# Kernel tuning notes

Measured on AMD Instinct MI355X. Metric: run time of the kernel, lower is better.

## Reference

```python
import jax, jax.numpy as jnp
import numpy as np

LEAF = 32
N = 262144          # num_nodes, power of 2
NLEV = 8            # HODLR levels
RANK = 16           # off-diagonal low-rank
NNZ = 1310720       # ~5 nnz per row


def setup_inputs() -> dict:
    key = jax.random.key(0)
    ks = jax.random.split(key, 24)
    inp = {}
    inp["leaf_blocks"] = jax.random.normal(ks[0], (1, N // LEAF, LEAF, LEAF), jnp.float32) * 0.1
    for l in range(NLEV):
        inp[f"u{l}"] = jax.random.normal(ks[1 + 2 * l], (1, N, RANK), jnp.float32) * 0.05
        inp[f"v{l}"] = jax.random.normal(ks[2 + 2 * l], (1, N, RANK), jnp.float32) * 0.05
    inp["A_indices"] = jax.random.randint(ks[17], (2, NNZ), 0, N, dtype=jnp.int32).astype(jnp.int64)
    inp["A_values"] = jax.random.normal(ks[18], (NNZ,), jnp.float32)
    inp["z"] = jax.random.normal(ks[19], (1, N, 1), jnp.float32)
    inp["num_nodes"] = N
    return inp


def apply_hodlr(leaf_blocks, factors, x, leaf_size=LEAF):
    # x: [B, n, 1]; leaf_blocks: [B, n/leaf, leaf, leaf]
    B, n, _ = x.shape
    nb = n // leaf_size
    xb = x.reshape(B, nb, leaf_size, 1)
    L = leaf_blocks
    # y = L @ (L^T @ x) + 1e-4 * x  per leaf block
    yb = jnp.matmul(L, jnp.matmul(jnp.swapaxes(L, -1, -2), xb)) + xb * 1e-4
    y = yb.reshape(B, n, 1)
    for li, (u, v) in enumerate(factors):
        num_splits = 2 ** (li + 1)
        bs = n // num_splits
        if bs == 0:
            continue
        npair = num_splits // 2
        vl = npair * 2 * bs  # == n for power-of-2 n
        xv = x[:, :vl].reshape(B, npair, 2, bs, 1)
        uv = u[:, :vl].reshape(B, npair, 2, bs, -1)
        vv = v[:, :vl].reshape(B, npair, 2, bs, -1)
        xL, xR = xv[:, :, 0], xv[:, :, 1]
        uL, uR = uv[:, :, 0], uv[:, :, 1]
        vL, vR = vv[:, :, 0], vv[:, :, 1]
        # cross-block low-rank updates: y_L += U_L (V_R^T x_R), y_R += U_R (V_L^T x_L)
        yL = jnp.matmul(uL, jnp.matmul(jnp.swapaxes(vR, -1, -2), xR))
        yR = jnp.matmul(uR, jnp.matmul(jnp.swapaxes(vL, -1, -2), xL))
        upd = jnp.stack([yL, yR], axis=2).reshape(B, vl, 1)
        if vl < n:
            upd = jnp.pad(upd, ((0, 0), (0, n - vl), (0, 0)))
        y = y + upd
    return y


def reference(leaf_blocks, u0, v0, u1, v1, u2, v2, u3, v3, u4, v4, u5, v5, u6, v6, u7, v7,
              A_indices, A_values, z, num_nodes):
    factors = [(u0, v0), (u1, v1), (u2, v2), (u3, v3),
               (u4, v4), (u5, v5), (u6, v6), (u7, v7)]
    w = apply_hodlr(leaf_blocks, factors, z)           # [1, N, 1]
    w_flat = w[0, :, 0]                                 # [N]
    rows, cols = A_indices[0], A_indices[1]
    # sparse COO matvec: y[r] = sum_k A_values[k] * w[cols[k]] over rows
    y_flat = jax.ops.segment_sum(A_values * w_flat[cols], rows, num_segments=num_nodes)
    y = y_flat.reshape(1, num_nodes, 1)
    return jnp.mean((y - z) ** 2)
```

## Files before the change

### kernel.cpp

```cpp
#include <hip/hip_runtime.h>

#define NN 262144
#define RANK 16
#define NNZ_K 1310720

struct P8 { const float* p[8]; };

__global__ __launch_bounds__(256) void k_levels_t(P8 v, const float* __restrict__ z,
                                                  float* __restrict__ tg) {
    __shared__ float zl[512];
    __shared__ float red[8][4][16];
    const int tid  = threadIdx.x;
    const int base = blockIdx.x * 512;

    zl[tid]       = z[base + tid];
    zl[tid + 256] = z[base + tid + 256];
    __syncthreads();

    const int q = tid & 3;
    const int e = tid >> 2;

    float4 acc[8];
#pragma unroll
    for (int l = 0; l < 8; ++l) acc[l] = make_float4(0.f, 0.f, 0.f, 0.f);

#pragma unroll
    for (int it = 0; it < 8; ++it) {
        const int jloc = it * 64 + e;
        const size_t j = (size_t)(base + jloc);
        const float zz = zl[jloc];
#pragma unroll
        for (int l = 0; l < 8; ++l) {
            const float4 vv = *(const float4*)(v.p[l] + j * RANK + q * 4);
            acc[l].x += vv.x * zz;
            acc[l].y += vv.y * zz;
            acc[l].z += vv.z * zz;
            acc[l].w += vv.w * zz;
        }
    }

    const int lane = tid & 63;
    const int wv   = tid >> 6;
#pragma unroll
    for (int l = 0; l < 8; ++l) {
        float4 a = acc[l];
#pragma unroll
        for (int m = 4; m <= 32; m <<= 1) {
            a.x += __shfl_xor(a.x, m);
            a.y += __shfl_xor(a.y, m);
            a.z += __shfl_xor(a.z, m);
            a.w += __shfl_xor(a.w, m);
        }
        if (lane < 4) *(float4*)&red[l][wv][lane * 4] = a;
    }
    __syncthreads();

    if (tid < 128) {
        const int l = tid >> 4;
        const int r = tid & 15;
        const float s = red[l][0][r] + red[l][1][r] + red[l][2][r] + red[l][3][r];
        const int h = base >> (17 - l);
        atomicAdd(&tg[(((2 << l) - 2) + h) * 16 + r], s);
    }
}

__global__ __launch_bounds__(256) void k_apply(const float* __restrict__ leaf, P8 u,
                                               const float* __restrict__ z,
                                               const float* __restrict__ tg,
                                               float* __restrict__ w) {
    __shared__ float Lp[8 * 1056];
    __shared__ float xl[256];
    __shared__ float t32[8][32];
    __shared__ float tl[8][16];

    const int tid  = threadIdx.x;
    const int base = blockIdx.x * 256;

    const float4* Lg = (const float4*)(leaf + (size_t)base * 32);
#pragma unroll
    for (int k = 0; k < 8; ++k) {
        const int fi = tid + k * 256;
        const float4 val = Lg[fi];
        const int lb  = fi >> 8;
        const int off = (fi & 255) * 4;
        const int row = off >> 5;
        const int col = off & 31;
        float* d = &Lp[lb * 1056 + row * 33 + col];
        d[0] = val.x; d[1] = val.y; d[2] = val.z; d[3] = val.w;
    }
    xl[tid] = z[base + tid];
    if (tid < 128) {
        const int l = tid >> 4;
        const int r = tid & 15;
        const int h = base >> (17 - l);
        tl[l][r] = tg[(((2 << l) - 2) + (h ^ 1)) * 16 + r];
    }
    __syncthreads();

    {
        const int lb = tid >> 5;
        const int c  = tid & 31;
        const float* Lb = &Lp[lb * 1056];
        const float* xb = &xl[lb * 32];
        float s = 0.f;
#pragma unroll
        for (int row = 0; row < 32; ++row)
            s += Lb[row * 33 + c] * xb[row];
        t32[lb][c] = s;
    }
    __syncthreads();

    {
        const int lb = tid >> 5;
        const int r  = tid & 31;
        const float* Lb = &Lp[lb * 1056 + r * 33];
        float acc = 1e-4f * xl[tid];
#pragma unroll
        for (int c = 0; c < 32; ++c)
            acc += Lb[c] * t32[lb][c];

        const size_t i = (size_t)(base + tid);
#pragma unroll
        for (int l = 0; l < 8; ++l) {
            const float4* up = (const float4*)(u.p[l] + i * RANK);
            const float4 a0 = up[0], a1 = up[1], a2 = up[2], a3 = up[3];
            acc += a0.x * tl[l][0]  + a0.y * tl[l][1]  + a0.z * tl[l][2]  + a0.w * tl[l][3]
                 + a1.x * tl[l][4]  + a1.y * tl[l][5]  + a1.z * tl[l][6]  + a1.w * tl[l][7]
                 + a2.x * tl[l][8]  + a2.y * tl[l][9]  + a2.z * tl[l][10] + a2.w * tl[l][11]
                 + a3.x * tl[l][12] + a3.y * tl[l][13] + a3.z * tl[l][14] + a3.w * tl[l][15];
        }
        w[i] = acc;
    }
}

__global__ __launch_bounds__(256) void k_spmv(const int* __restrict__ idx,
                                              const float* __restrict__ vals,
                                              const float* __restrict__ w,
                                              float* __restrict__ y) {
    const int k = blockIdx.x * 256 + threadIdx.x;
    const int row = idx[k];
    const int col = idx[NNZ_K + k];
    atomicAdd(&y[row], vals[k] * w[col]);
}

__global__ __launch_bounds__(256) void k_loss(const float* __restrict__ y,
                                              const float* __restrict__ z,
                                              float* __restrict__ loss) {
    const int i = blockIdx.x * 256 + threadIdx.x;
    const float d = y[i] - z[i];
    float s = d * d;
#pragma unroll
    for (int m = 32; m >= 1; m >>= 1) s += __shfl_down(s, m);
    __shared__ float r4[4];
    const int lane = threadIdx.x & 63, wv = threadIdx.x >> 6;
    if (lane == 0) r4[wv] = s;
    __syncthreads();
    if (threadIdx.x == 0) atomicAdd(loss, r4[0] + r4[1] + r4[2] + r4[3]);
}

__global__ void k_fin(const float* __restrict__ loss, float* __restrict__ out) {
    out[0] = loss[0] * (1.0f / (float)NN);
}

extern "C" void kernel_launch(void* const* d_in, const int* in_sizes, int n_in,
                              void* d_out, int out_size, void* d_ws, size_t ws_size,
                              hipStream_t stream) {
    const float* leaf = (const float*)d_in[0];
    P8 u, v;
    for (int l = 0; l < 8; ++l) {
        u.p[l] = (const float*)d_in[1 + 2 * l];
        v.p[l] = (const float*)d_in[2 + 2 * l];
    }
    const int*   Aidx  = (const int*)d_in[17];
    const float* Avals = (const float*)d_in[18];
    const float* z     = (const float*)d_in[19];

    float* ws   = (float*)d_ws;
    float* tg   = ws;
    float* loss = ws + 8192;
    float* y    = ws + 16384;
    float* w    = ws + 16384 + NN;

    hipMemsetAsync(d_ws, 0, (size_t)(16384 + NN) * sizeof(float), stream);

    k_levels_t<<<NN / 512, 256, 0, stream>>>(v, z, tg);
    k_apply  <<<NN / 256, 256, 0, stream>>>(leaf, u, z, tg, w);
    k_spmv   <<<NNZ_K / 256, 256, 0, stream>>>(Aidx, Avals, w, y);
    k_loss   <<<NN / 256, 256, 0, stream>>>(y, z, loss);
    k_fin    <<<1, 1, 0, stream>>>(loss, (float*)d_out);
}
```

Before: 396.7 us.

## Replace atomic level reductions with partial buffers and drop workspace memset

The level projection kernel now writes per-block partial sums to a buffer, and a new small kernel reduces them deterministically into the level vectors, zeroing the loss accumulator as it goes. Clearing y moves into the apply kernel, so the workspace memset is removed. The SpMV and loss kernels now handle four elements per thread using vector loads. This trades contended atomics and a memset for one extra kernel launch.

```diff
diff --git a/kernel.cpp b/kernel.cpp
--- a/kernel.cpp
+++ b/kernel.cpp
@@ -7,7 +7,7 @@
 struct P8 { const float* p[8]; };
 
 __global__ __launch_bounds__(256) void k_levels_t(P8 v, const float* __restrict__ z,
-                                                  float* __restrict__ tg) {
+                                                  float* __restrict__ part) {
     __shared__ float zl[512];
     __shared__ float red[8][4][16];
     const int tid  = threadIdx.x;
@@ -59,15 +59,39 @@
         const int l = tid >> 4;
         const int r = tid & 15;
         const float s = red[l][0][r] + red[l][1][r] + red[l][2][r] + red[l][3][r];
-        const int h = base >> (17 - l);
-        atomicAdd(&tg[(((2 << l) - 2) + h) * 16 + r], s);
-    }
+        part[(l * 512 + blockIdx.x) * 16 + r] = s;
+    }
+}
+
+__global__ __launch_bounds__(64) void k_reduce_t(const float* __restrict__ part,
+                                                 float* __restrict__ tg,
+                                                 float* __restrict__ loss) {
+    const int b = blockIdx.x;
+    if (b == 0 && threadIdx.x == 0) loss[0] = 0.f;
+    const int t = b + 2;
+    const int l = 30 - __clz(t);
+    const int h = t - (2 << l);
+    const int cnt = 256 >> l;
+    const int c0  = h * cnt;
+    const int r = threadIdx.x & 15;
+    const int g = threadIdx.x >> 4;
+
+    float s = 0.f;
+    for (int c = c0 + g; c < c0 + cnt; c += 4)
+        s += part[(l * 512 + c) * 16 + r];
+
+    __shared__ float red[64];
+    red[threadIdx.x] = s;
+    __syncthreads();
+    if (threadIdx.x < 16)
+        tg[((2 << l) - 2 + h) * 16 + r] = red[r] + red[16 + r] + red[32 + r] + red[48 + r];
 }
 
 __global__ __launch_bounds__(256) void k_apply(const float* __restrict__ leaf, P8 u,
                                                const float* __restrict__ z,
                                                const float* __restrict__ tg,
-                                               float* __restrict__ w) {
+                                               float* __restrict__ w,
+                                               float* __restrict__ y) {
     __shared__ float Lp[8 * 1056];
     __shared__ float xl[256];
     __shared__ float t32[8][32];
@@ -130,6 +154,7 @@
                  + a3.x * tl[l][12] + a3.y * tl[l][13] + a3.z * tl[l][14] + a3.w * tl[l][15];
         }
         w[i] = acc;
+        y[i] = 0.f;
     }
 }
 
@@ -137,18 +162,24 @@
                                               const float* __restrict__ vals,
                                               const float* __restrict__ w,
                                               float* __restrict__ y) {
-    const int k = blockIdx.x * 256 + threadIdx.x;
-    const int row = idx[k];
-    const int col = idx[NNZ_K + k];
-    atomicAdd(&y[row], vals[k] * w[col]);
+    const int k = (blockIdx.x * 256 + threadIdx.x) * 4;
+    const int4   r4 = *(const int4*)(idx + k);
+    const int4   c4 = *(const int4*)(idx + NNZ_K + k);
+    const float4 v4 = *(const float4*)(vals + k);
+    atomicAdd(&y[r4.x], v4.x * w[c4.x]);
+    atomicAdd(&y[r4.y], v4.y * w[c4.y]);
+    atomicAdd(&y[r4.z], v4.z * w[c4.z]);
+    atomicAdd(&y[r4.w], v4.w * w[c4.w]);
 }
 
 __global__ __launch_bounds__(256) void k_loss(const float* __restrict__ y,
                                               const float* __restrict__ z,
                                               float* __restrict__ loss) {
     const int i = blockIdx.x * 256 + threadIdx.x;
-    const float d = y[i] - z[i];
-    float s = d * d;
+    const float4 a = ((const float4*)y)[i];
+    const float4 b = ((const float4*)z)[i];
+    const float dx = a.x - b.x, dy = a.y - b.y, dz = a.z - b.z, dw = a.w - b.w;
+    float s = dx * dx + dy * dy + dz * dz + dw * dw;
 #pragma unroll
     for (int m = 32; m >= 1; m >>= 1) s += __shfl_down(s, m);
     __shared__ float r4[4];
@@ -176,16 +207,16 @@
     const float* z     = (const float*)d_in[19];
 
     float* ws   = (float*)d_ws;
-    float* tg   = ws;
-    float* loss = ws + 8192;
-    float* y    = ws + 16384;
-    float* w    = ws + 16384 + NN;
-
-    hipMemsetAsync(d_ws, 0, (size_t)(16384 + NN) * sizeof(float), stream);
-
-    k_levels_t<<<NN / 512, 256, 0, stream>>>(v, z, tg);
-    k_apply  <<<NN / 256, 256, 0, stream>>>(leaf, u, z, tg, w);
-    k_spmv   <<<NNZ_K / 256, 256, 0, stream>>>(Aidx, Avals, w, y);
-    k_loss   <<<NN / 256, 256, 0, stream>>>(y, z, loss);
+    float* part = ws;
+    float* tg   = ws + 65536;
+    float* loss = ws + 73728;
+    float* y    = ws + 81920;
+    float* w    = ws + 81920 + NN;
+
+    k_levels_t<<<NN / 512, 256, 0, stream>>>(v, z, part);
+    k_reduce_t<<<510, 64, 0, stream>>>(part, tg, loss);
+    k_apply  <<<NN / 256, 256, 0, stream>>>(leaf, u, z, tg, w, y);
+    k_spmv   <<<NNZ_K / 1024, 256, 0, stream>>>(Aidx, Avals, w, y);
+    k_loss   <<<NN / 1024, 256, 0, stream>>>(y, z, loss);
     k_fin    <<<1, 1, 0, stream>>>(loss, (float*)d_out);
 }
```

After: 401.8 us. Within noise of the previous version (+1.3%).
